# Kernel tuning notes

Hardware: AMD Instinct MI355X
Metric: run time of the kernel (lower is better)

## Reference

```python
import jax, jax.numpy as jnp
import numpy as np

NUM_HEADS = 8


def setup_inputs() -> dict:
    key = jax.random.key(0)
    ks = jax.random.split(key, 8)
    B, S, D = 2, 4096, 512
    # Linear weights init uniform(-0.1, 0.1), no bias; stored as [in, out]
    u = lambda k, shp: jax.random.uniform(k, shp, jnp.float32, -0.1, 0.1)
    return {
        "query_antecedent": jax.random.normal(ks[0], (B, S, D), jnp.float32),
        "memory_antecedent": jax.random.normal(ks[1], (B, S, D), jnp.float32),
        "bias": jax.random.normal(ks[2], (1, S, S), jnp.float32),
        "Wq": u(ks[3], (D, D)),
        "Wk": u(ks[4], (D, D)),
        "Wv": u(ks[5], (D, D)),
        "Wo": u(ks[6], (D, D)),
    }


def reference(query_antecedent, memory_antecedent, bias, Wq, Wk, Wv, Wo):
    B, S, D = query_antecedent.shape
    H = NUM_HEADS
    hd = D // H
    scale = hd ** (-0.5)
    q = (query_antecedent @ Wq) * scale              # [B,S,D]
    k = memory_antecedent @ Wk                       # [B,S,D]
    v = memory_antecedent @ Wv                       # [B,S,D]
    q = q.reshape(B, S, H, hd)
    k = k.reshape(B, S, H, hd)
    v = v.reshape(B, S, H, hd)
    # per-head logits with shared bias (broadcast over batch and heads)
    logits = jnp.einsum("bqhd,bkhd->bhqk", q, k) + bias[:, None, :, :]
    weights = jax.nn.softmax(logits, axis=-1)        # [B,H,S,S]
    out = jnp.einsum("bhqk,bkhd->bqhd", weights, v).reshape(B, S, D)
    return out @ Wo
```

## Files before the change

### kernel.cpp

```cpp
#include <hip/hip_runtime.h>
#include <hip/hip_bf16.h>

typedef __attribute__((ext_vector_type(8))) __bf16 bf16x8;
typedef __attribute__((ext_vector_type(4))) __bf16 bf16x4;
typedef __attribute__((ext_vector_type(4))) float f32x4;
typedef __attribute__((ext_vector_type(2))) unsigned u32x2;
typedef __attribute__((ext_vector_type(4))) unsigned u32x4;

#define LOG2E 1.4426950408889634f
#define FIXED_M 16.0f

static __device__ __forceinline__ f32x4 mfma16(bf16x8 a, bf16x8 b, f32x4 c) {
  return __builtin_amdgcn_mfma_f32_16x16x32_bf16(a, b, c, 0, 0, 0);
}

static __device__ __forceinline__ void gload_lds16(const void* g, void* l) {
  __builtin_amdgcn_global_load_lds(
      (const __attribute__((address_space(1))) unsigned int*)g,
      (__attribute__((address_space(3))) unsigned int*)l, 16, 0, 0);
}

__global__ __launch_bounds__(256) void k_cvt(const float* __restrict__ in,
                                             __bf16* __restrict__ out, int n4) {
  for (int i = blockIdx.x * blockDim.x + threadIdx.x; i < n4;
       i += gridDim.x * blockDim.x) {
    float4 v = reinterpret_cast<const float4*>(in)[i];
    bf16x4 o = {(__bf16)v.x, (__bf16)v.y, (__bf16)v.z, (__bf16)v.w};
    reinterpret_cast<bf16x4*>(out)[i] = o;
  }
}

__global__ __launch_bounds__(256) void k_wt(const float* __restrict__ W,
                                            __bf16* __restrict__ Wt) {
  __shared__ float tile[64][65];
  int bx = blockIdx.x;
  int by = blockIdx.y;
  int tid = threadIdx.x;
#pragma unroll
  for (int p = 0; p < 16; p++) {
    int idx = p * 256 + tid;
    int r = idx >> 6, c = idx & 63;
    tile[r][c] = W[(size_t)(by * 64 + r) * 512 + bx * 64 + c];
  }
  __syncthreads();
#pragma unroll
  for (int p = 0; p < 16; p++) {
    int idx = p * 256 + tid;
    int rn = idx >> 6, ck = idx & 63;
    Wt[(size_t)(bx * 64 + rn) * 512 + by * 64 + ck] = (__bf16)tile[ck][rn];
  }
}

template <int OUT_MODE>
__global__ __launch_bounds__(256) void k_gemm(const __bf16* __restrict__ A,
                                              const __bf16* __restrict__ Bt,
                                              void* __restrict__ Cout,
                                              float scale) {
  constexpr bool SWAP = (OUT_MODE != 2);
  __shared__ __bf16 As[128][72];
  __shared__ __bf16 Bs[64][72];
  const int tid = threadIdx.x;
  const int wid = tid >> 6, lane = tid & 63;
  const int g = lane >> 4, c = lane & 15;
  const int m0 = blockIdx.x * 128, n0 = blockIdx.y * 64;
  const int wr = wid >> 1, wc = wid & 1;

  f32x4 acc[4][2];
#pragma unroll
  for (int i = 0; i < 4; i++)
#pragma unroll
    for (int j = 0; j < 2; j++) acc[i][j] = (f32x4){0.f, 0.f, 0.f, 0.f};

  for (int k0 = 0; k0 < 512; k0 += 64) {
#pragma unroll
    for (int q = 0; q < 4; q++) {
      int idx = (q * 256 + tid) * 8;
      int r = idx >> 6, cc = idx & 63;
      bf16x8 v = *reinterpret_cast<const bf16x8*>(A + (size_t)(m0 + r) * 512 + k0 + cc);
      *reinterpret_cast<bf16x8*>(&As[r][cc]) = v;
    }
#pragma unroll
    for (int q = 0; q < 2; q++) {
      int idx = (q * 256 + tid) * 8;
      int r = idx >> 6, cc = idx & 63;
      bf16x8 v = *reinterpret_cast<const bf16x8*>(Bt + (size_t)(n0 + r) * 512 + k0 + cc);
      *reinterpret_cast<bf16x8*>(&Bs[r][cc]) = v;
    }
    __syncthreads();
#pragma unroll
    for (int kk = 0; kk < 2; kk++) {
      bf16x8 bfrag[2];
#pragma unroll
      for (int nf = 0; nf < 2; nf++)
        bfrag[nf] = *reinterpret_cast<const bf16x8*>(&Bs[wc * 32 + nf * 16 + c][kk * 32 + g * 8]);
#pragma unroll
      for (int mf = 0; mf < 4; mf++) {
        bf16x8 afrag = *reinterpret_cast<const bf16x8*>(&As[wr * 64 + mf * 16 + c][kk * 32 + g * 8]);
#pragma unroll
        for (int nf = 0; nf < 2; nf++)
          acc[mf][nf] = SWAP ? mfma16(bfrag[nf], afrag, acc[mf][nf])
                             : mfma16(afrag, bfrag[nf], acc[mf][nf]);
      }
    }
    __syncthreads();
  }
#pragma unroll
  for (int mf = 0; mf < 4; mf++)
#pragma unroll
    for (int nf = 0; nf < 2; nf++) {
      if (OUT_MODE == 0) {
        int mm = m0 + wr * 64 + mf * 16 + c;
        int nnb = n0 + wc * 32 + nf * 16 + g * 4;
        int b = mm >> 12, s = mm & 4095, h = nnb >> 6, d = nnb & 63;
        bf16x4 ov = {(__bf16)(acc[mf][nf][0] * scale), (__bf16)(acc[mf][nf][1] * scale),
                     (__bf16)(acc[mf][nf][2] * scale), (__bf16)(acc[mf][nf][3] * scale)};
        *reinterpret_cast<bf16x4*>((__bf16*)Cout + ((((size_t)b * 8 + h) * 4096) + s) * 64 + d) = ov;
      } else if (OUT_MODE == 1) {
        int mm = m0 + wr * 64 + mf * 16 + c;
        int nnb = n0 + wc * 32 + nf * 16 + g * 4;
        f32x4 ov = acc[mf][nf] * scale;
        *reinterpret_cast<f32x4*>((float*)Cout + (size_t)mm * 512 + nnb) = ov;
      } else {
        int mmb = m0 + wr * 64 + mf * 16 + g * 4;
        int nn = n0 + wc * 32 + nf * 16 + c;
        int b = mmb >> 12, s = mmb & 4095, h = nn >> 6, d = nn & 63;
        bf16x4 ov = {(__bf16)(acc[mf][nf][0] * scale), (__bf16)(acc[mf][nf][1] * scale),
                     (__bf16)(acc[mf][nf][2] * scale), (__bf16)(acc[mf][nf][3] * scale)};
        *reinterpret_cast<bf16x4*>((__bf16*)Cout + (((size_t)b * 8 + h) * 64 + d) * 4096 + s) = ov;
      }
    }
}

__global__ __launch_bounds__(256, 2) void k_attn(const __bf16* __restrict__ Q,
                                                 const __bf16* __restrict__ K,
                                                 const __bf16* __restrict__ Vt,
                                                 const float* __restrict__ bias,
                                                 __bf16* __restrict__ Out) {
  __shared__ __bf16 KVs[2][2][2][64][64];

  const int id = blockIdx.x;
  const int qb = ((id >> 6) << 3) | (id & 7);
  const int h = (id >> 3) & 7;
  const int tid = threadIdx.x, wid = tid >> 6, lane = tid & 63;
  const int g = lane >> 4, c = lane & 15;
  const int swz = (c & 7) << 4;
  const char* KbP[2] = {(const char*)(K + (size_t)h * 4096 * 64),
                        (const char*)(K + (size_t)(8 + h) * 4096 * 64)};
  const char* VbP[2] = {(const char*)(Vt + (size_t)h * 64 * 4096),
                        (const char*)(Vt + (size_t)(8 + h) * 64 * 4096)};
  const int q0 = qb * 64 + wid * 16;
  const int myq = q0 + c;

  auto stage = [&](int db, int chunk) {
    const int bt = wid >> 1, reg = wid & 1;
    char* dst0 = (char*)&KVs[db][bt][reg][0][0];
#pragma unroll
    for (int j = 0; j < 8; j++) {
      int Lp = j * 1024 + lane * 16;
      int L = Lp ^ (((Lp >> 7) & 7) << 4);
      const char* src = (reg == 0)
          ? KbP[bt] + (size_t)chunk * 8192 + L
          : VbP[bt] + (size_t)(L >> 7) * 8192 + (size_t)chunk * 128 + (L & 127);
      gload_lds16(src, dst0 + j * 1024);
    }
  };

  const float* brow = bias + (size_t)myq * 4096;

#define LOADB(dst, chunk)                                                      \
  {                                                                            \
    _Pragma("unroll") for (int f = 0; f < 4; f++) dst[f] =                     \
        *reinterpret_cast<const f32x4*>(brow + (chunk) * 64 + f * 16 + g * 4); \
  }

  bf16x8 qa[2][2];
  {
    const __bf16* Qh0 = Q + (size_t)h * 4096 * 64;
    const __bf16* Qh1 = Q + (size_t)(8 + h) * 4096 * 64;
    qa[0][0] = *reinterpret_cast<const bf16x8*>(Qh0 + (size_t)myq * 64 + g * 8);
    qa[0][1] = *reinterpret_cast<const bf16x8*>(Qh0 + (size_t)myq * 64 + 32 + g * 8);
    qa[1][0] = *reinterpret_cast<const bf16x8*>(Qh1 + (size_t)myq * 64 + g * 8);
    qa[1][1] = *reinterpret_cast<const bf16x8*>(Qh1 + (size_t)myq * 64 + 32 + g * 8);
  }

  f32x4 lacc[2];
  lacc[0] = (f32x4){0.f, 0.f, 0.f, 0.f};
  lacc[1] = (f32x4){0.f, 0.f, 0.f, 0.f};
  f32x4 o[2][4];
#pragma unroll
  for (int bt = 0; bt < 2; bt++)
#pragma unroll
    for (int f = 0; f < 4; f++) o[bt][f] = (f32x4){0.f, 0.f, 0.f, 0.f};

  f32x4 bA[4], bB[4];
  const float NM = -FIXED_M * LOG2E;

  auto process = [&](int db, f32x4 (&bv)[4]) {
    asm volatile("s_waitcnt vmcnt(12)" ::: "memory");
    __builtin_amdgcn_s_barrier();
#pragma unroll
    for (int bt = 0; bt < 2; bt++) {
      const char* Kl = (const char*)&KVs[db][bt][0][0][0];
      const char* Vl = (const char*)&KVs[db][bt][1][0][0];
      f32x4 st[4];
      __builtin_amdgcn_s_setprio(1);
#pragma unroll
      for (int f = 0; f < 4; f++) {
        const char* rb = Kl + (f * 16 + c) * 128;
        bf16x8 k0 = *reinterpret_cast<const bf16x8*>(rb + ((g * 16) ^ swz));
        bf16x8 k1 = *reinterpret_cast<const bf16x8*>(rb + ((64 + g * 16) ^ swz));
        st[f] = mfma16(k1, qa[bt][1], mfma16(k0, qa[bt][0], bv[f]));
      }
      __builtin_amdgcn_s_setprio(0);
      bf16x8 vf[2][4];
#pragma unroll
      for (int kk = 0; kk < 2; kk++)
#pragma unroll
        for (int fd = 0; fd < 4; fd++) {
          const char* rb = Vl + (fd * 16 + c) * 128;
          u32x2 lo = *reinterpret_cast<const u32x2*>(rb + ((kk * 64 + g * 8) ^ swz));
          u32x2 hi = *reinterpret_cast<const u32x2*>(rb + ((kk * 64 + 32 + g * 8) ^ swz));
          u32x4 w = {lo[0], lo[1], hi[0], hi[1]};
          vf[kk][fd] = __builtin_bit_cast(bf16x8, w);
        }
#pragma unroll
      for (int f = 0; f < 4; f++) {
#pragma unroll
        for (int r = 0; r < 4; r++)
          st[f][r] = __builtin_exp2f(__builtin_fmaf(st[f][r], LOG2E, NM));
        lacc[bt] += st[f];
      }
      __builtin_amdgcn_s_setprio(1);
#pragma unroll
      for (int kk = 0; kk < 2; kk++) {
        bf16x8 pf = {(__bf16)st[2 * kk][0],     (__bf16)st[2 * kk][1],
                     (__bf16)st[2 * kk][2],     (__bf16)st[2 * kk][3],
                     (__bf16)st[2 * kk + 1][0], (__bf16)st[2 * kk + 1][1],
                     (__bf16)st[2 * kk + 1][2], (__bf16)st[2 * kk + 1][3]};
#pragma unroll
        for (int fd = 0; fd < 4; fd++)
          o[bt][fd] = mfma16(vf[kk][fd], pf, o[bt][fd]);
      }
      __builtin_amdgcn_s_setprio(0);
    }
    __builtin_amdgcn_s_barrier();
  };

  stage(0, 0);
  asm volatile("" ::: "memory");
  stage(1, 1);
  asm volatile("" ::: "memory");
  LOADB(bA, 0);
  asm volatile("" ::: "memory");
  LOADB(bB, 1);
  asm volatile("" ::: "memory");

  for (int t = 0; t < 64; t += 2) {
    process(0, bA);
    stage(0, (t + 2) & 63);
    asm volatile("" ::: "memory");
    LOADB(bA, ((t + 2) & 63));
    asm volatile("" ::: "memory");
    process(1, bB);
    stage(1, (t + 3) & 63);
    asm volatile("" ::: "memory");
    LOADB(bB, ((t + 3) & 63));
    asm volatile("" ::: "memory");
  }

#pragma unroll
  for (int bt = 0; bt < 2; bt++) {
    float l = lacc[bt][0] + lacc[bt][1] + lacc[bt][2] + lacc[bt][3];
    l += __shfl_xor(l, 16);
    l += __shfl_xor(l, 32);
    float inv = 1.f / l;
    __bf16* Orow = Out + ((size_t)bt * 4096 + myq) * 512 + h * 64;
#pragma unroll
    for (int fd = 0; fd < 4; fd++) {
      bf16x4 ov = {(__bf16)(o[bt][fd][0] * inv), (__bf16)(o[bt][fd][1] * inv),
                   (__bf16)(o[bt][fd][2] * inv), (__bf16)(o[bt][fd][3] * inv)};
      *reinterpret_cast<bf16x4*>(Orow + fd * 16 + g * 4) = ov;
    }
  }
#undef LOADB
}

extern "C" void kernel_launch(void* const* d_in, const int* in_sizes, int n_in,
                              void* d_out, int out_size, void* d_ws, size_t ws_size,
                              hipStream_t stream) {
  const float* xq = (const float*)d_in[0];
  const float* xm = (const float*)d_in[1];
  const float* bias = (const float*)d_in[2];
  const float* Wq = (const float*)d_in[3];
  const float* Wk = (const float*)d_in[4];
  const float* Wv = (const float*)d_in[5];
  const float* Wo = (const float*)d_in[6];

  const size_t MB = 1024 * 1024;
  char* ws = (char*)d_ws;
  __bf16* xq_b = (__bf16*)(ws + 0);
  __bf16* xm_b = (__bf16*)(ws + 8 * MB);
  __bf16* wqt = (__bf16*)(ws + 16 * MB);
  __bf16* wkt = (__bf16*)(ws + 16 * MB + 524288);
  __bf16* wvt = (__bf16*)(ws + 17 * MB);
  __bf16* wot = (__bf16*)(ws + 17 * MB + 524288);
  __bf16* Qb = (__bf16*)(ws + 18 * MB);
  __bf16* Kb = (__bf16*)(ws + 26 * MB);
  __bf16* AOb = (__bf16*)(ws + 34 * MB);
  __bf16* Vtb = (__bf16*)(ws + 42 * MB);
  if (ws_size < 50 * MB) return;

  const int n4 = 8192 * 512 / 4;
  k_cvt<<<2048, 256, 0, stream>>>(xq, xq_b, n4);
  k_cvt<<<2048, 256, 0, stream>>>(xm, xm_b, n4);
  k_wt<<<dim3(8, 8), 256, 0, stream>>>(Wq, wqt);
  k_wt<<<dim3(8, 8), 256, 0, stream>>>(Wk, wkt);
  k_wt<<<dim3(8, 8), 256, 0, stream>>>(Wv, wvt);
  k_wt<<<dim3(8, 8), 256, 0, stream>>>(Wo, wot);

  k_gemm<0><<<dim3(64, 8), 256, 0, stream>>>(xq_b, wqt, Qb, 0.125f);
  k_gemm<0><<<dim3(64, 8), 256, 0, stream>>>(xm_b, wkt, Kb, 1.0f);
  k_gemm<2><<<dim3(64, 8), 256, 0, stream>>>(xm_b, wvt, Vtb, 1.0f);

  k_attn<<<512, 256, 0, stream>>>(Qb, Kb, Vtb, bias, AOb);

  k_gemm<1><<<dim3(64, 8), 256, 0, stream>>>(AOb, wot, d_out, 1.0f);
}
```

Before: 229.3 us.

## Batch conversion/transpose launches and load GEMM tiles via direct-to-LDS swizzled loads

Merges the two input conversion kernels into one launch and the four weight-transpose kernels into a single 3D-grid launch, cutting launch overhead. The projection GEMM now fills shared memory with global_load_lds 16-byte direct loads into an unpadded tile with an XOR swizzle. The swizzle replaces the padding as the way to avoid LDS bank conflicts, and the direct loads skip the register round trip. The attention kernel, which dominates runtime, is unchanged, so the gains are limited to the surrounding kernels.

```diff
diff --git a/kernel.cpp b/kernel.cpp
--- a/kernel.cpp
+++ b/kernel.cpp
@@ -20,19 +20,34 @@
       (__attribute__((address_space(3))) unsigned int*)l, 16, 0, 0);
 }
 
-__global__ __launch_bounds__(256) void k_cvt(const float* __restrict__ in,
-                                             __bf16* __restrict__ out, int n4) {
-  for (int i = blockIdx.x * blockDim.x + threadIdx.x; i < n4;
+__global__ __launch_bounds__(256) void k_cvt2(const float* __restrict__ a,
+                                              const float* __restrict__ b,
+                                              __bf16* __restrict__ oa,
+                                              __bf16* __restrict__ ob, int n4each) {
+  int total = 2 * n4each;
+  for (int i = blockIdx.x * blockDim.x + threadIdx.x; i < total;
        i += gridDim.x * blockDim.x) {
-    float4 v = reinterpret_cast<const float4*>(in)[i];
+    const float* src = (i < n4each) ? a : b;
+    __bf16* dst = (i < n4each) ? oa : ob;
+    int j = (i < n4each) ? i : i - n4each;
+    float4 v = reinterpret_cast<const float4*>(src)[j];
     bf16x4 o = {(__bf16)v.x, (__bf16)v.y, (__bf16)v.z, (__bf16)v.w};
-    reinterpret_cast<bf16x4*>(out)[i] = o;
-  }
-}
-
-__global__ __launch_bounds__(256) void k_wt(const float* __restrict__ W,
-                                            __bf16* __restrict__ Wt) {
+    reinterpret_cast<bf16x4*>(dst)[j] = o;
+  }
+}
+
+__global__ __launch_bounds__(256) void k_wt4(const float* __restrict__ W0,
+                                             const float* __restrict__ W1,
+                                             const float* __restrict__ W2,
+                                             const float* __restrict__ W3,
+                                             __bf16* __restrict__ T0,
+                                             __bf16* __restrict__ T1,
+                                             __bf16* __restrict__ T2,
+                                             __bf16* __restrict__ T3) {
   __shared__ float tile[64][65];
+  const int z = blockIdx.z;
+  const float* W = (z == 0) ? W0 : (z == 1) ? W1 : (z == 2) ? W2 : W3;
+  __bf16* Wt = (z == 0) ? T0 : (z == 1) ? T1 : (z == 2) ? T2 : T3;
   int bx = blockIdx.x;
   int by = blockIdx.y;
   int tid = threadIdx.x;
@@ -57,13 +72,16 @@
                                               void* __restrict__ Cout,
                                               float scale) {
   constexpr bool SWAP = (OUT_MODE != 2);
-  __shared__ __bf16 As[128][72];
-  __shared__ __bf16 Bs[64][72];
+  __shared__ __bf16 As[128][64];
+  __shared__ __bf16 Bs[64][64];
   const int tid = threadIdx.x;
   const int wid = tid >> 6, lane = tid & 63;
   const int g = lane >> 4, c = lane & 15;
+  const int swz = (c & 7) << 4;
   const int m0 = blockIdx.x * 128, n0 = blockIdx.y * 64;
   const int wr = wid >> 1, wc = wid & 1;
+  const char* Ab = (const char*)A;
+  const char* Bb = (const char*)Bt;
 
   f32x4 acc[4][2];
 #pragma unroll
@@ -73,29 +91,34 @@
 
   for (int k0 = 0; k0 < 512; k0 += 64) {
 #pragma unroll
-    for (int q = 0; q < 4; q++) {
-      int idx = (q * 256 + tid) * 8;
-      int r = idx >> 6, cc = idx & 63;
-      bf16x8 v = *reinterpret_cast<const bf16x8*>(A + (size_t)(m0 + r) * 512 + k0 + cc);
-      *reinterpret_cast<bf16x8*>(&As[r][cc]) = v;
-    }
-#pragma unroll
-    for (int q = 0; q < 2; q++) {
-      int idx = (q * 256 + tid) * 8;
-      int r = idx >> 6, cc = idx & 63;
-      bf16x8 v = *reinterpret_cast<const bf16x8*>(Bt + (size_t)(n0 + r) * 512 + k0 + cc);
-      *reinterpret_cast<bf16x8*>(&Bs[r][cc]) = v;
+    for (int p = 0; p < 4; p++) {
+      int Lp = p * 4096 + tid * 16;
+      int L = Lp ^ (((Lp >> 7) & 7) << 4);
+      gload_lds16(Ab + (size_t)(m0 + (L >> 7)) * 1024 + k0 * 2 + (L & 127),
+                  (char*)As + Lp);
+    }
+#pragma unroll
+    for (int p = 0; p < 2; p++) {
+      int Lp = p * 4096 + tid * 16;
+      int L = Lp ^ (((Lp >> 7) & 7) << 4);
+      gload_lds16(Bb + (size_t)(n0 + (L >> 7)) * 1024 + k0 * 2 + (L & 127),
+                  (char*)Bs + Lp);
     }
     __syncthreads();
 #pragma unroll
     for (int kk = 0; kk < 2; kk++) {
       bf16x8 bfrag[2];
 #pragma unroll
-      for (int nf = 0; nf < 2; nf++)
-        bfrag[nf] = *reinterpret_cast<const bf16x8*>(&Bs[wc * 32 + nf * 16 + c][kk * 32 + g * 8]);
+      for (int nf = 0; nf < 2; nf++) {
+        int row = wc * 32 + nf * 16 + c;
+        bfrag[nf] = *reinterpret_cast<const bf16x8*>(
+            (const char*)Bs + row * 128 + ((kk * 64 + g * 16) ^ swz));
+      }
 #pragma unroll
       for (int mf = 0; mf < 4; mf++) {
-        bf16x8 afrag = *reinterpret_cast<const bf16x8*>(&As[wr * 64 + mf * 16 + c][kk * 32 + g * 8]);
+        int row = wr * 64 + mf * 16 + c;
+        bf16x8 afrag = *reinterpret_cast<const bf16x8*>(
+            (const char*)As + row * 128 + ((kk * 64 + g * 16) ^ swz));
 #pragma unroll
         for (int nf = 0; nf < 2; nf++)
           acc[mf][nf] = SWAP ? mfma16(bfrag[nf], afrag, acc[mf][nf])
@@ -311,12 +334,8 @@
   if (ws_size < 50 * MB) return;
 
   const int n4 = 8192 * 512 / 4;
-  k_cvt<<<2048, 256, 0, stream>>>(xq, xq_b, n4);
-  k_cvt<<<2048, 256, 0, stream>>>(xm, xm_b, n4);
-  k_wt<<<dim3(8, 8), 256, 0, stream>>>(Wq, wqt);
-  k_wt<<<dim3(8, 8), 256, 0, stream>>>(Wk, wkt);
-  k_wt<<<dim3(8, 8), 256, 0, stream>>>(Wv, wvt);
-  k_wt<<<dim3(8, 8), 256, 0, stream>>>(Wo, wot);
+  k_cvt2<<<4096, 256, 0, stream>>>(xq, xm, xq_b, xm_b, n4);
+  k_wt4<<<dim3(8, 8, 4), 256, 0, stream>>>(Wq, Wk, Wv, Wo, wqt, wkt, wvt, wot);
 
   k_gemm<0><<<dim3(64, 8), 256, 0, stream>>>(xq_b, wqt, Qb, 0.125f);
   k_gemm<0><<<dim3(64, 8), 256, 0, stream>>>(xm_b, wkt, Kb, 1.0f);
```

Measured after the change: 217.5 us. 1.05x faster.
